# Kernel optimization log

Hardware: AMD Instinct MI355X
Metric: run time of the kernel (lower is better)

Reference implementation:

```python
import jax, jax.numpy as jnp
import numpy as np

H = 16          # num heads
BUCKETS = 256   # position_buckets -> pos_ebd_size (att_span)
MAX_REL = 512   # max_relative_positions


def _log_bucket(rel, bucket_size, max_position):
    mid = bucket_size // 2
    sign = jnp.sign(rel).astype(jnp.float32)
    abs_pos = jnp.where((rel < mid) & (rel > -mid), mid - 1, jnp.abs(rel)).astype(jnp.float32)
    log_pos = jnp.ceil(jnp.log(abs_pos / mid) / np.log((max_position - 1) / mid) * (mid - 1)) + mid
    bucket = jnp.where(abs_pos <= mid, rel.astype(jnp.float32), log_pos * sign)
    return bucket.astype(jnp.int32)


def _rel_pos(seq_len):
    ids = jnp.arange(seq_len)
    rel = ids[:, None] - ids[None, :]
    return _log_bucket(rel, BUCKETS, MAX_REL)  # [S,S] int32 in [-span, span]


def setup_inputs() -> dict:
    key = jax.random.key(0)
    ks = jax.random.split(key, 16)
    B, S, D = 4, 1024, 1024
    K2 = 2 * BUCKETS
    s = 0.02
    def lin(k, din, dout):
        return jax.random.normal(k, (din, dout), jnp.float32) * s
    return {
        "hidden_states": jax.random.normal(ks[0], (B, S, D), jnp.float32),
        "Wq": lin(ks[1], D, D), "bq": jnp.zeros((D,), jnp.float32),
        "Wk": lin(ks[2], D, D), "bk": jnp.zeros((D,), jnp.float32),
        "Wv": lin(ks[3], D, D), "bv": jnp.zeros((D,), jnp.float32),
        "Wo": lin(ks[4], D, D), "bo": jnp.zeros((D,), jnp.float32),
        "rel_emb": jax.random.normal(ks[5], (K2, D), jnp.float32) * s,
        "ln_g": jnp.ones((D,), jnp.float32), "ln_b": jnp.zeros((D,), jnp.float32),
        "Wpk": lin(ks[6], D, D), "bpk": jnp.zeros((D,), jnp.float32),
        "Wpq": lin(ks[7], D, D), "bpq": jnp.zeros((D,), jnp.float32),
    }


def reference(hidden_states, Wq, bq, Wk, bk, Wv, bv, Wo, bo,
              rel_emb, ln_g, ln_b, Wpk, bpk, Wpq, bpq):
    B, S, D = hidden_states.shape
    hd = D // H
    span = BUCKETS

    def shape_heads(x):  # [*, L, D] -> [*, H, L, hd]
        return x.reshape(*x.shape[:-1], H, hd).swapaxes(-2, -3)

    q = shape_heads(hidden_states @ Wq + bq)  # [B,H,S,hd]
    k = shape_heads(hidden_states @ Wk + bk)
    v = shape_heads(hidden_states @ Wv + bv)

    scale_factor = 3  # 1 + c2p + p2c
    scores = jnp.einsum('bhsd,bhkd->bhsk', q, k) / jnp.sqrt(jnp.float32(hd * scale_factor))

    # relative embeddings: LayerNorm over feature dim
    mu = rel_emb.mean(-1, keepdims=True)
    var = rel_emb.var(-1, keepdims=True)
    re = (rel_emb - mu) / jnp.sqrt(var + 1e-5) * ln_g + ln_b  # [2K, D]

    pos_k = shape_heads(re @ Wpk + bpk)  # [H, 2K, hd]
    pos_q = shape_heads(re @ Wpq + bpq)  # [H, 2K, hd]

    rel = _rel_pos(S)  # [S,S]
    bias_scale = jnp.sqrt(jnp.float32(hd * 2))

    # content-to-position
    c2p = jnp.einsum('bhsd,hkd->bhsk', q, pos_k)  # [B,H,S,2K]
    c2p_idx = jnp.clip(rel + span, 0, 2 * span - 1)  # [S,S]
    c2p = jnp.take_along_axis(c2p, jnp.broadcast_to(c2p_idx[None, None], (B, H, S, S)), axis=-1)
    scores = scores + c2p / bias_scale

    # position-to-content
    p2c = jnp.einsum('bhsd,hkd->bhsk', k, pos_q)  # [B,H,S,2K]
    p2c_idx = jnp.clip(-rel + span, 0, 2 * span - 1)
    p2c = jnp.take_along_axis(p2c, jnp.broadcast_to(p2c_idx[None, None], (B, H, S, S)), axis=-1)
    scores = scores + p2c.swapaxes(-1, -2) / bias_scale

    probs = jax.nn.softmax(scores.astype(jnp.float32), axis=-1).astype(q.dtype)
    ctx = jnp.einsum('bhsk,bhkd->bhsd', probs, v)  # [B,H,S,hd]
    ctx = ctx.swapaxes(1, 2).reshape(B, S, D)
    return ctx @ Wo + bo
```

## Files before the change

kernel.cpp:

```cpp
#include <hip/hip_runtime.h>

typedef unsigned short u16;
typedef __attribute__((ext_vector_type(8))) short short8_t;
typedef __attribute__((ext_vector_type(4))) float floatx4;

typedef const void __attribute__((address_space(1)))* gas_ptr;
typedef void __attribute__((address_space(3)))* las_ptr;

__device__ __forceinline__ float bf2f(u16 u){
  union { unsigned i; float f; } v; v.i = ((unsigned)u) << 16; return v.f;
}
__device__ __forceinline__ u16 f2bf(float x){
  unsigned u = __float_as_uint(x);
  return (u16)((u + 0x7FFFu + ((u >> 16) & 1u)) >> 16);
}
__device__ __forceinline__ int bucket_idx(int delta){
  int b;
  if (delta >= -128 && delta <= 128) b = delta;
  else {
    float a = (float)(delta < 0 ? -delta : delta);
    float lp = ceilf(logf(a * (1.0f / 128.0f)) / logf(511.0f / 128.0f) * 127.0f) + 128.0f;
    b = (int)lp;
    if (delta < 0) b = -b;
  }
  int idx = b + 256;
  return idx < 0 ? 0 : (idx > 511 ? 511 : idx);
}
__device__ __forceinline__ int win_lo(int s0, int t){
  int dlo = s0 - t * 64 - 63;
  int lo = bucket_idx(dlo) & ~1;
  return lo > 384 ? 384 : lo;
}

__global__ __launch_bounds__(256) void k_prep(
    const float* __restrict__ hs,
    const float* __restrict__ W0, const float* __restrict__ W1, const float* __restrict__ W2,
    const float* __restrict__ W3, const float* __restrict__ W4, const float* __restrict__ W5,
    const float* __restrict__ rel, const float* __restrict__ lng, const float* __restrict__ lnb,
    const float* __restrict__ bq, const float* __restrict__ bk, const float* __restrict__ bv,
    const float* __restrict__ bpk, const float* __restrict__ bpq,
    u16* __restrict__ h_bf, u16* __restrict__ Wt5, u16* __restrict__ Wo_t,
    u16* __restrict__ re_bf, u16* __restrict__ idxt,
    float* __restrict__ qkvb, float* __restrict__ posb)
{
  __shared__ float t[64][65];
  const int bid = blockIdx.x, tid = threadIdx.x;
  if (bid < 4096){
    int i = bid * 256 + tid;
    float4 v = ((const float4*)hs)[i];
    ushort4 o;
    o.x = f2bf(v.x); o.y = f2bf(v.y); o.z = f2bf(v.z); o.w = f2bf(v.w);
    ((ushort4*)h_bf)[i] = o;
  } else if (bid < 5632){
    int b2 = bid - 4096;
    int z = b2 >> 8, rem = b2 & 255;
    const float* W = (z == 0) ? W0 : (z == 1) ? W1 : (z == 2) ? W2 : (z == 3) ? W3 : (z == 4) ? W4 : W5;
    u16* Wt = (z < 5) ? (Wt5 + (long)z * 1048576) : Wo_t;
    int n0 = (rem & 15) * 64, k0 = (rem >> 4) * 64;
    #pragma unroll
    for (int i = 0; i < 16; i++){
      int e = i * 256 + tid; int r = e >> 6, c = e & 63;
      t[r][c] = W[(long)(k0 + r) * 1024 + n0 + c];
    }
    __syncthreads();
    #pragma unroll
    for (int i = 0; i < 16; i++){
      int e = i * 256 + tid; int r = e >> 6, c = e & 63;
      Wt[(long)(n0 + r) * 1024 + k0 + c] = f2bf(t[c][r]);
    }
  } else if (bid < 6144){
    int row = bid - 5632;
    float* red = (float*)t;
    float4 v = ((const float4*)(rel + (long)row * 1024))[tid];
    float s  = v.x + v.y + v.z + v.w;
    float s2 = v.x*v.x + v.y*v.y + v.z*v.z + v.w*v.w;
    #pragma unroll
    for (int o = 1; o < 64; o <<= 1){ s += __shfl_xor(s, o); s2 += __shfl_xor(s2, o); }
    if ((tid & 63) == 0){ red[(tid >> 6) * 2] = s; red[(tid >> 6) * 2 + 1] = s2; }
    __syncthreads();
    s  = red[0] + red[2] + red[4] + red[6];
    s2 = red[1] + red[3] + red[5] + red[7];
    float mu  = s * (1.f / 1024.f);
    float var = s2 * (1.f / 1024.f) - mu * mu;
    float rs  = rsqrtf(var + 1e-5f);
    float4 gg = ((const float4*)lng)[tid];
    float4 bb = ((const float4*)lnb)[tid];
    ushort4 o;
    o.x = f2bf((v.x - mu) * rs * gg.x + bb.x);
    o.y = f2bf((v.y - mu) * rs * gg.y + bb.y);
    o.z = f2bf((v.z - mu) * rs * gg.z + bb.z);
    o.w = f2bf((v.w - mu) * rs * gg.w + bb.w);
    ((ushort4*)(re_bf + (long)row * 1024))[tid] = o;
  } else {
    for (int i = tid; i < 2048; i += 256)
      idxt[i] = (u16)bucket_idx(i - 1024);
    for (int i = tid; i < 1024; i += 256){
      qkvb[i] = bq[i]; qkvb[1024 + i] = bk[i]; qkvb[2048 + i] = bv[i];
      posb[i] = bpk[i]; posb[1024 + i] = bpq[i];
    }
  }
}

template<int MODE>
__global__ __launch_bounds__(256) void k_gemm(
    const u16* __restrict__ A, const u16* __restrict__ Bt,
    const float* __restrict__ bias, void* __restrict__ C, void* __restrict__ C2,
    int M, int N, int K, int lda, int ldb)
{
  __shared__ __attribute__((aligned(16))) u16 smem[16384];
  u16* As = smem;
  u16* Bs = smem + 8192;
  const int z = blockIdx.z;
  const u16* Ab = A;
  const u16* Bb = Bt;
  if (MODE == 3){ Bb = Bt + (long)z * 1048576; bias += z << 10; }
  if (MODE == 4){ Ab = A + (long)z * 65536; Bb = Bt + (long)(z >> 6) * 524288 + (long)(z & 15) * 32768; }
  const int m0 = blockIdx.y * 128, n0 = blockIdx.x * 128;
  const int tid = threadIdx.x, lane = tid & 63, w = tid >> 6;
  const int wm = (w >> 1) * 64, wn = (w & 1) * 64;
  floatx4 acc[4][4];
  #pragma unroll
  for (int i = 0; i < 4; i++)
    #pragma unroll
    for (int j = 0; j < 4; j++) acc[i][j] = (floatx4){0.f, 0.f, 0.f, 0.f};

  const int r8 = lane >> 3;
  const int cswz = ((lane & 7) ^ r8) << 4;

  for (int kt = 0; kt < K; kt += 64){
    #pragma unroll
    for (int c = 0; c < 4; c++){
      int row = (c * 4 + w) * 8 + r8;
      const char* ga = (const char*)(Ab + (long)(m0 + row) * lda + kt) + cswz;
      __builtin_amdgcn_global_load_lds((gas_ptr)ga, (las_ptr)((char*)As + (c * 4 + w) * 1024), 16, 0, 0);
      const char* gb = (const char*)(Bb + (long)(n0 + row) * ldb + kt) + cswz;
      __builtin_amdgcn_global_load_lds((gas_ptr)gb, (las_ptr)((char*)Bs + (c * 4 + w) * 1024), 16, 0, 0);
    }
    __syncthreads();
    short8_t af[2][4], bfr[2][4];
    #pragma unroll
    for (int kk = 0; kk < 2; kk++){
      #pragma unroll
      for (int i = 0; i < 4; i++){
        int ra = wm + i * 16 + (lane & 15);
        af[kk][i] = *(const short8_t*)((const char*)As + ra * 128 + ((kk * 64 + ((lane >> 4) << 4)) ^ ((ra & 7) << 4)));
        int rb = wn + i * 16 + (lane & 15);
        bfr[kk][i] = *(const short8_t*)((const char*)Bs + rb * 128 + ((kk * 64 + ((lane >> 4) << 4)) ^ ((rb & 7) << 4)));
      }
    }
    #pragma unroll
    for (int i = 0; i < 4; i++)
      #pragma unroll
      for (int j = 0; j < 4; j++){
        acc[i][j] = __builtin_amdgcn_mfma_f32_16x16x32_bf16(af[0][i], bfr[0][j], acc[i][j], 0, 0, 0);
        acc[i][j] = __builtin_amdgcn_mfma_f32_16x16x32_bf16(af[1][i], bfr[1][j], acc[i][j], 0, 0, 0);
      }
    __syncthreads();
  }

  if (MODE == 0){
    float* fs = (float*)smem;
    #pragma unroll
    for (int h = 0; h < 2; h++){
      if ((w & 1) == h){
        #pragma unroll
        for (int i = 0; i < 4; i++)
          #pragma unroll
          for (int j = 0; j < 4; j++)
            #pragma unroll
            for (int r = 0; r < 4; r++){
              int ml = wm + i * 16 + ((lane >> 4) << 2) + r;
              int nl = j * 16 + (lane & 15);
              fs[ml * 64 + (nl ^ (((ml >> 2) & 3) << 4))] = acc[i][j][r] + bias[n0 + h * 64 + nl];
            }
      }
      __syncthreads();
      const int row16 = tid >> 4, cch = tid & 15;
      #pragma unroll
      for (int rr = 0; rr < 8; rr++){
        int ml = rr * 16 + row16;
        float4 vv = *(const float4*)&fs[ml * 64 + ((cch * 4) ^ (((ml >> 2) & 3) << 4))];
        *(float4*)((float*)C + (long)(m0 + ml) * N + n0 + h * 64 + cch * 4) = vv;
      }
      __syncthreads();
    }
    return;
  }

  if (MODE == 4){
    #pragma unroll
    for (int i = 0; i < 4; i++){
      #pragma unroll
      for (int j = 0; j < 4; j++){
        #pragma unroll
        for (int r = 0; r < 4; r++){
          int ml = wm + i * 16 + ((lane >> 4) << 2) + r;
          int nl = wn + j * 16 + (lane & 15);
          int byte_ = ml * 256 + ((nl * 2) ^ ((ml & 7) << 4));
          *(u16*)((char*)smem + byte_) = f2bf(exp2f(acc[i][j][r] * 0.12751743f));
        }
      }
    }
    __syncthreads();
    const int row16 = tid >> 4, cch = tid & 15;
    #pragma unroll
    for (int rr = 0; rr < 8; rr++){
      int ml = rr * 16 + row16;
      short8_t vv = *(const short8_t*)((const char*)smem + ml * 256 + ((cch * 16) ^ ((ml & 7) << 4)));
      *(short8_t*)((u16*)C + (long)z * 524288 + (long)(m0 + ml) * 512 + n0 + cch * 8) = vv;
    }
    return;
  }

  if (MODE == 5){
    if (n0 >= 2048){
      #pragma unroll
      for (int i = 0; i < 4; i++){
        #pragma unroll
        for (int j = 0; j < 4; j++){
          #pragma unroll
          for (int r = 0; r < 4; r++){
            int ml = wm + i * 16 + ((lane >> 4) << 2) + r;
            int nl = wn + j * 16 + (lane & 15);
            float v = acc[i][j][r] + bias[n0 + nl];
            int byte_ = nl * 256 + ((ml * 2) ^ ((nl & 7) << 4));
            *(u16*)((char*)smem + byte_) = f2bf(v);
          }
        }
      }
      __syncthreads();
      #pragma unroll
      for (int rr = 0; rr < 8; rr++){
        int nl = rr * 16 + (tid >> 4);
        int np = n0 + nl - 2048;
        int mc = tid & 15;
        short8_t vv = *(const short8_t*)((const char*)smem + nl * 256 + ((mc * 16) ^ ((nl & 7) << 4)));
        int m = m0 + mc * 8;
        long base = ((long)((m >> 10) * 16 + (np >> 6)) * 64 + (np & 63)) * 1024 + (m & 1023);
        *(short8_t*)((u16*)C2 + base) = vv;
      }
    } else {
      #pragma unroll
      for (int i = 0; i < 4; i++){
        #pragma unroll
        for (int j = 0; j < 4; j++){
          #pragma unroll
          for (int r = 0; r < 4; r++){
            int ml = wm + i * 16 + ((lane >> 4) << 2) + r;
            int nl = wn + j * 16 + (lane & 15);
            float v = acc[i][j][r] + bias[n0 + nl];
            int byte_ = ml * 256 + ((nl * 2) ^ ((ml & 7) << 4));
            *(u16*)((char*)smem + byte_) = f2bf(v);
          }
        }
      }
      __syncthreads();
      const int row16 = tid >> 4, cch = tid & 15;
      const int mat = n0 >> 10;
      u16* Cd = (u16*)C + (long)mat * 4194304;
      #pragma unroll
      for (int rr = 0; rr < 8; rr++){
        int ml = rr * 16 + row16;
        short8_t vv = *(const short8_t*)((const char*)smem + ml * 256 + ((cch * 16) ^ ((ml & 7) << 4)));
        int m = m0 + ml;
        int np = (n0 & 1023) + cch * 8;
        long base = ((long)((m >> 10) * 16 + (np >> 6)) * 1024 + (m & 1023)) * 64 + (np & 63);
        *(short8_t*)(Cd + base) = vv;
      }
    }
    return;
  }

  #pragma unroll
  for (int i = 0; i < 4; i++){
    #pragma unroll
    for (int j = 0; j < 4; j++){
      #pragma unroll
      for (int r = 0; r < 4; r++){
        int m = m0 + wm + i * 16 + ((lane >> 4) << 2) + r;
        int n = n0 + wn + j * 16 + (lane & 15);
        float v = acc[i][j][r] + bias[n];
        ((u16*)C)[(long)z * 524288 + ((long)(n >> 6) * 512 + m) * 64 + (n & 63)] = f2bf(v);
      }
    }
  }
}

__global__ __launch_bounds__(256, 2) void k_bias(
    const u16* __restrict__ EC, const u16* __restrict__ EP,
    const u16* __restrict__ T3, u16* __restrict__ EB, int bhbase)
{
  __shared__ __attribute__((aligned(16))) u16 C2W[2][8192];
  __shared__ __attribute__((aligned(16))) u16 P2W[2][8192];
  __shared__ __attribute__((aligned(16))) u16 IDW[2][128];
  const int flat0 = blockIdx.x;
  const int chunk = gridDim.x >> 3;
  const int flat = (flat0 & 7) * chunk + (flat0 >> 3);
  const int bhl = flat >> 5;
  const int sb  = (flat >> 1) & 15;
  const int kq  = flat & 1;
  const int bh = bhbase + bhl;
  const int tid = threadIdx.x, lane = tid & 63, w = tid >> 6;
  const int s0 = sb * 64;
  const u16* c2b = EC + (long)bh * 524288;
  const u16* p2b = EP + (long)bh * 524288;
  u16* EBb = EB + ((long)bhl << 20);

  const int r2 = tid >> 2;
  const int q2 = tid & 3;
  const int c2key = (r2 & 15) << 4;

  auto STAGE = [&](int buf, int t){
    const int ixlo = win_lo(s0, t);
    const int k0 = t * 64;
    #pragma unroll
    for (int r = 0; r < 16; r++){
      int row = w * 16 + r;
      const char* sa = (const char*)(c2b + (long)(s0 + row) * 512 + ixlo) + ((lane * 4) ^ ((row & 15) << 4));
      __builtin_amdgcn_global_load_lds((gas_ptr)sa, (las_ptr)((char*)&C2W[buf][0] + row * 256), 4, 0, 0);
      const char* sp = (const char*)(p2b + (long)(k0 + row) * 512 + ixlo) + ((lane * 4) ^ ((row & 15) << 4));
      __builtin_amdgcn_global_load_lds((gas_ptr)sp, (las_ptr)((char*)&P2W[buf][0] + row * 256), 4, 0, 0);
    }
    if (w == 3){
      int dev = s0 - k0 - 64;
      __builtin_amdgcn_global_load_lds((gas_ptr)((const char*)(T3 + (dev + 1024)) + lane * 4),
                                       (las_ptr)((char*)&IDW[buf][0]), 4, 0, 0);
    }
  };

  const int t0 = kq * 8;
  STAGE(0, t0);
  asm volatile("s_waitcnt vmcnt(0)" ::: "memory");
  __builtin_amdgcn_s_barrier();

  for (int i = 0; i < 8; i++){
    const int t = t0 + i, buf = i & 1;
    const int k0 = t * 64;
    const int ixlo = win_lo(s0, t);

    if (i < 7) STAGE(buf ^ 1, t + 1);

    u16 ov[16];
    #pragma unroll
    for (int c = 0; c < 16; c++){
      int kl = q2 * 16 + c;
      int j = r2 - kl + 64;
      int ix = (int)IDW[buf][j];
      int x = (ix - ixlo) * 2;
      float b1 = bf2f(*(const u16*)((const char*)&C2W[buf][0] + r2 * 256 + (x ^ c2key)));
      float b2 = bf2f(*(const u16*)((const char*)&P2W[buf][0] + kl * 256 + (x ^ ((kl & 15) << 4))));
      ov[c] = f2bf(b1 * b2);
    }
    u16* dst = EBb + (((long)(s0 + r2)) << 10) + k0 + q2 * 16;
    uint4 st0, st1;
    st0.x = (unsigned)ov[0]  | ((unsigned)ov[1]  << 16);
    st0.y = (unsigned)ov[2]  | ((unsigned)ov[3]  << 16);
    st0.z = (unsigned)ov[4]  | ((unsigned)ov[5]  << 16);
    st0.w = (unsigned)ov[6]  | ((unsigned)ov[7]  << 16);
    st1.x = (unsigned)ov[8]  | ((unsigned)ov[9]  << 16);
    st1.y = (unsigned)ov[10] | ((unsigned)ov[11] << 16);
    st1.z = (unsigned)ov[12] | ((unsigned)ov[13] << 16);
    st1.w = (unsigned)ov[14] | ((unsigned)ov[15] << 16);
    *(uint4*)dst = st0;
    *(uint4*)(dst + 8) = st1;

    if (i < 7){
      asm volatile("s_waitcnt vmcnt(2)" ::: "memory");
      __builtin_amdgcn_s_barrier();
    }
  }
}

__global__ __launch_bounds__(256, 3) void k_attn_eb(
    const u16* __restrict__ Q, const u16* __restrict__ K, const u16* __restrict__ Vt,
    const u16* __restrict__ EB, u16* __restrict__ ctx, int bhbase)
{
  __shared__ __attribute__((aligned(16))) u16 Ks[2][4096];
  __shared__ __attribute__((aligned(16))) u16 Vs[2][4096];
  __shared__ __attribute__((aligned(16))) u16 EBs[4096];
  __shared__ __attribute__((aligned(16))) u16 Pt[4096];
  const int flat0 = blockIdx.x;
  const int chunk = gridDim.x >> 3;
  const int flat = (flat0 & 7) * chunk + (flat0 >> 3);
  const int bhl = flat >> 4, sb = flat & 15;
  const int bh = bhbase + bhl;
  const int tid = threadIdx.x, lane = tid & 63, w = tid >> 6;
  const int s15 = lane & 15, g = lane >> 4;
  const int s0 = sb * 64;
  const int myrow = w * 16 + s15;
  const int s_row = s0 + myrow;
  const u16* Qb  = Q   + (long)bh * 65536;
  const u16* Kg  = K   + (long)bh * 65536;
  const u16* Vg  = Vt  + (long)bh * 65536;
  const u16* EBg = EB  + ((long)bhl << 20);

  short8_t qf0 = *(const short8_t*)(Qb + (long)s_row * 64 + g * 8);
  short8_t qf1 = *(const short8_t*)(Qb + (long)s_row * 64 + 32 + g * 8);

  const int srow8  = lane >> 3;
  const int schunk = (lane & 7) ^ srow8;
  const float sA2 = 0.10411754f;

  auto STAGE_KV = [&](int buf, int kt){
    #pragma unroll
    for (int ii = 0; ii < 2; ii++){
      int i = w * 2 + ii;
      int row = i * 8 + srow8;
      __builtin_amdgcn_global_load_lds(
        (gas_ptr)((const char*)(Kg + (long)(kt + row) * 64) + schunk * 16),
        (las_ptr)((char*)&Ks[buf][0] + i * 1024), 16, 0, 0);
      __builtin_amdgcn_global_load_lds(
        (gas_ptr)((const char*)(Vg + (long)row * 1024 + kt) + schunk * 16),
        (las_ptr)((char*)&Vs[buf][0] + i * 1024), 16, 0, 0);
    }
  };
  auto STAGE_EB = [&](int kt){
    #pragma unroll
    for (int ii = 0; ii < 2; ii++){
      int rowl = w * 16 + ii * 8 + srow8;
      const char* src = (const char*)(EBg + (((long)(s0 + rowl)) << 10) + kt) + schunk * 16;
      __builtin_amdgcn_global_load_lds((gas_ptr)src,
        (las_ptr)((char*)EBs + (w * 2 + ii) * 1024), 16, 0, 0);
    }
  };

  STAGE_KV(0, 0);
  STAGE_EB(0);

  float rowsum = 0.f;
  floatx4 oacc[4];
  #pragma unroll
  for (int dt = 0; dt < 4; dt++) oacc[dt] = (floatx4){0.f, 0.f, 0.f, 0.f};

  const int psw = (myrow & 7) << 4;

  for (int t = 0; t < 16; t++){
    const int buf = t & 1;
    const int kt = t * 64;

    asm volatile("s_waitcnt vmcnt(2)" ::: "memory");
    asm volatile("s_waitcnt lgkmcnt(0)" ::: "memory");
    __builtin_amdgcn_s_barrier();

    STAGE_KV(buf ^ 1, (t < 15) ? kt + 64 : 0);

    floatx4 a[4];
    #pragma unroll
    for (int T = 0; T < 4; T++){
      int row = T * 16 + s15;
      const char* rp = (const char*)&Ks[buf][0] + row * 128;
      int sw = (row & 7) << 4;
      short8_t k0v = *(const short8_t*)(rp + ((g * 16) ^ sw));
      short8_t k1v = *(const short8_t*)(rp + ((64 + g * 16) ^ sw));
      floatx4 acc = (floatx4){0.f, 0.f, 0.f, 0.f};
      acc = __builtin_amdgcn_mfma_f32_16x16x32_bf16(k0v, qf0, acc, 0, 0, 0);
      acc = __builtin_amdgcn_mfma_f32_16x16x32_bf16(k1v, qf1, acc, 0, 0, 0);
      a[T] = acc;
    }

    asm volatile("s_waitcnt vmcnt(4)" ::: "memory");

    #pragma unroll
    for (int T = 0; T < 4; T++){
      uint2 ebv = *(const uint2*)((const char*)EBs + myrow * 128 + ((T * 32 + g * 8) ^ psw));
      float e0 = exp2f(a[T][0] * sA2) * bf2f((u16)(ebv.x & 0xffff));
      float e1 = exp2f(a[T][1] * sA2) * bf2f((u16)(ebv.x >> 16));
      float e2 = exp2f(a[T][2] * sA2) * bf2f((u16)(ebv.y & 0xffff));
      float e3 = exp2f(a[T][3] * sA2) * bf2f((u16)(ebv.y >> 16));
      u16 p0 = f2bf(e0), p1 = f2bf(e1), p2v = f2bf(e2), p3 = f2bf(e3);
      rowsum += (bf2f(p0) + bf2f(p1)) + (bf2f(p2v) + bf2f(p3));
      uint2 pk2;
      pk2.x = (unsigned)p0  | ((unsigned)p1 << 16);
      pk2.y = (unsigned)p2v | ((unsigned)p3 << 16);
      *(uint2*)((char*)Pt + myrow * 128 + ((T * 32 + g * 8) ^ psw)) = pk2;
    }

    asm volatile("s_waitcnt lgkmcnt(0)" ::: "memory");
    STAGE_EB((t < 15) ? kt + 64 : 0);

    #pragma unroll
    for (int M = 0; M < 2; M++){
      short8_t pf = *(const short8_t*)((const char*)Pt + myrow * 128 + ((M * 64 + g * 16) ^ psw));
      #pragma unroll
      for (int dt = 0; dt < 4; dt++){
        int drow = dt * 16 + s15;
        short8_t vf = *(const short8_t*)((const char*)&Vs[buf][0] + drow * 128 + ((M * 64 + g * 16) ^ ((drow & 7) << 4)));
        oacc[dt] = __builtin_amdgcn_mfma_f32_16x16x32_bf16(pf, vf, oacc[dt], 0, 0, 0);
      }
    }
  }

  asm volatile("s_waitcnt vmcnt(0)" ::: "memory");

  rowsum += __shfl_xor(rowsum, 16);
  rowsum += __shfl_xor(rowsum, 32);
  float rinv = 1.f / rowsum;

  const int b = bh >> 4, h = bh & 15;
  #pragma unroll
  for (int r = 0; r < 4; r++){
    float ri = __shfl(rinv, g * 4 + r);
    int s_out = s0 + w * 16 + g * 4 + r;
    #pragma unroll
    for (int dt = 0; dt < 4; dt++){
      long oi = ((long)b * 1024 + s_out) * 1024 + h * 64 + dt * 16 + s15;
      ctx[oi] = f2bf(oacc[dt][r] * ri);
    }
  }
}

extern "C" void kernel_launch(void* const* d_in, const int* in_sizes, int n_in,
                              void* d_out, int out_size, void* d_ws, size_t ws_size,
                              hipStream_t stream){
  const float* hs  = (const float*)d_in[0];
  const float* Wq  = (const float*)d_in[1];
  const float* bq  = (const float*)d_in[2];
  const float* Wk  = (const float*)d_in[3];
  const float* bk  = (const float*)d_in[4];
  const float* Wv  = (const float*)d_in[5];
  const float* bv  = (const float*)d_in[6];
  const float* Wo  = (const float*)d_in[7];
  const float* bo  = (const float*)d_in[8];
  const float* rel = (const float*)d_in[9];
  const float* lng = (const float*)d_in[10];
  const float* lnb = (const float*)d_in[11];
  const float* Wpk = (const float*)d_in[12];
  const float* bpk = (const float*)d_in[13];
  const float* Wpq = (const float*)d_in[14];
  const float* bpq = (const float*)d_in[15];

  char* ws = (char*)d_ws;
  size_t off = 0;
  auto alloc = [&](size_t bytes){ size_t o = off; off += (bytes + 255) & ~(size_t)255; return o; };
  u16* Wo_t  = (u16*)(ws + alloc(1048576UL * 2));
  u16* Qd    = (u16*)(ws + alloc(4194304UL * 2));
  u16* Kd    = (u16*)(ws + alloc(4194304UL * 2));
  u16* Vtd   = (u16*)(ws + alloc(4194304UL * 2));
  u16* ECd   = (u16*)(ws + alloc(33554432UL * 2));
  u16* EPd   = (u16*)(ws + alloc(33554432UL * 2));
  u16* ctx   = (u16*)(ws + alloc(4194304UL * 2));
  u16* idxt  = (u16*)(ws + alloc(2048UL * 2));
  float* qkvb = (float*)(ws + alloc(3072UL * 4));
  float* posb = (float*)(ws + alloc(2048UL * 4));
  size_t dead0 = off;
  u16* h_bf  = (u16*)(ws + alloc(4194304UL * 2));
  u16* Wt5   = (u16*)(ws + alloc(5UL * 1048576 * 2));
  u16* re_bf = (u16*)(ws + alloc(524288UL * 2));
  u16* posk  = (u16*)(ws + alloc(524288UL * 2));
  u16* posq  = (u16*)(ws + alloc(524288UL * 2));
  u16* EB    = (u16*)(ws + dead0);
  const bool full = (ws_size >= dead0 + 134217728UL);
  (void)posq; (void)Kd;

  k_prep<<<6145, 256, 0, stream>>>(hs, Wq, Wk, Wv, Wpk, Wpq, Wo, rel, lng, lnb,
                                   bq, bk, bv, bpk, bpq,
                                   h_bf, Wt5, Wo_t, re_bf, idxt, qkvb, posb);

  k_gemm<5><<<dim3(24, 32, 1), 256, 0, stream>>>(h_bf, Wt5, qkvb, Qd, Vtd,
                                                 4096, 3072, 1024, 1024, 1024);
  k_gemm<3><<<dim3(8, 4, 2), 256, 0, stream>>>(re_bf, Wt5 + 3145728, posb, posk, nullptr,
                                               512, 1024, 1024, 1024, 1024);
  k_gemm<4><<<dim3(4, 8, 128), 256, 0, stream>>>(Qd, posk, nullptr, ECd, nullptr,
                                                 1024, 512, 64, 64, 64);

  if (full){
    k_bias   <<<dim3(2048), 256, 0, stream>>>(ECd, EPd, idxt, EB, 0);
    k_attn_eb<<<dim3(1024), 256, 0, stream>>>(Qd, Kd, Vtd, EB, ctx, 0);
  } else {
    k_bias   <<<dim3(1024), 256, 0, stream>>>(ECd, EPd, idxt, EB, 0);
    k_attn_eb<<<dim3(512),  256, 0, stream>>>(Qd, Kd, Vtd, EB, ctx, 0);
    k_bias   <<<dim3(1024), 256, 0, stream>>>(ECd, EPd, idxt, EB, 32);
    k_attn_eb<<<dim3(512),  256, 0, stream>>>(Qd, Kd, Vtd, EB, ctx, 32);
  }

  k_gemm<0><<<dim3(8, 32, 1), 256, 0, stream>>>(ctx, Wo_t, bo, d_out, nullptr,
                                                4096, 1024, 1024, 1024, 1024);
}
```

Before: 277.9 us.

## Fuse positional projection GEMM into QKV GEMM launch and remap tile order

The separate launch for the relative-embedding projection (pos_k/pos_q) is folded into the QKV projection kernel by adding extra grid rows that take the positional path, with surplus blocks exiting early. This removes one kernel launch and lets the small positional GEMM fill idle CUs alongside the large GEMM. The QKV and output-projection GEMMs also remap block IDs into a strided order meant to improve L2 locality across XCDs. Risks: the added branching and early-exit blocks, plus a different tile ordering that could change cache behaviour.

```diff
diff --git a/kernel.cpp b/kernel.cpp
--- a/kernel.cpp
+++ b/kernel.cpp
@@ -105,17 +105,46 @@
 __global__ __launch_bounds__(256) void k_gemm(
     const u16* __restrict__ A, const u16* __restrict__ Bt,
     const float* __restrict__ bias, void* __restrict__ C, void* __restrict__ C2,
-    int M, int N, int K, int lda, int ldb)
+    int M, int N, int K, int lda, int ldb,
+    const u16* __restrict__ Apos, const float* __restrict__ biaspos, void* __restrict__ Cpos)
 {
   __shared__ __attribute__((aligned(16))) u16 smem[16384];
   u16* As = smem;
   u16* Bs = smem + 8192;
+  const int bx = blockIdx.x, by = blockIdx.y;
   const int z = blockIdx.z;
   const u16* Ab = A;
   const u16* Bb = Bt;
-  if (MODE == 3){ Bb = Bt + (long)z * 1048576; bias += z << 10; }
-  if (MODE == 4){ Ab = A + (long)z * 65536; Bb = Bt + (long)(z >> 6) * 524288 + (long)(z & 15) * 32768; }
-  const int m0 = blockIdx.y * 128, n0 = blockIdx.x * 128;
+  const float* biasv = bias;
+  bool pospath = false;
+  int pz = 0;
+  int m0, n0;
+  if (MODE == 5){
+    if (by >= 32){
+      if (bx >= 16) return;
+      pospath = true;
+      pz = bx >> 3;
+      Ab = Apos;
+      Bb = Bt + 3145728 + (long)pz * 1048576;
+      biasv = biaspos + (pz << 10);
+      m0 = (by - 32) * 128;
+      n0 = (bx & 7) * 128;
+    } else {
+      int bid = by * 24 + bx;
+      int nf = (bid & 7) * 96 + (bid >> 3);
+      m0 = (nf / 24) * 128;
+      n0 = (nf % 24) * 128;
+    }
+  } else if (MODE == 0){
+    int bid = by * 8 + bx;
+    int nf = (bid & 7) * 32 + (bid >> 3);
+    m0 = (nf >> 3) * 128;
+    n0 = (nf & 7) * 128;
+  } else {
+    if (MODE == 4){ Ab = A + (long)z * 65536; Bb = Bt + (long)(z >> 6) * 524288 + (long)(z & 15) * 32768; }
+    m0 = by * 128;
+    n0 = bx * 128;
+  }
   const int tid = threadIdx.x, lane = tid & 63, w = tid >> 6;
   const int wm = (w >> 1) * 64, wn = (w & 1) * 64;
   floatx4 acc[4][4];
@@ -171,7 +200,7 @@
             for (int r = 0; r < 4; r++){
               int ml = wm + i * 16 + ((lane >> 4) << 2) + r;
               int nl = j * 16 + (lane & 15);
-              fs[ml * 64 + (nl ^ (((ml >> 2) & 3) << 4))] = acc[i][j][r] + bias[n0 + h * 64 + nl];
+              fs[ml * 64 + (nl ^ (((ml >> 2) & 3) << 4))] = acc[i][j][r] + biasv[n0 + h * 64 + nl];
             }
       }
       __syncthreads();
@@ -213,6 +242,22 @@
   }
 
   if (MODE == 5){
+    if (pospath){
+      #pragma unroll
+      for (int i = 0; i < 4; i++){
+        #pragma unroll
+        for (int j = 0; j < 4; j++){
+          #pragma unroll
+          for (int r = 0; r < 4; r++){
+            int m = m0 + wm + i * 16 + ((lane >> 4) << 2) + r;
+            int n = n0 + wn + j * 16 + (lane & 15);
+            float v = acc[i][j][r] + biasv[n];
+            ((u16*)Cpos)[(long)pz * 524288 + ((long)(n >> 6) * 512 + m) * 64 + (n & 63)] = f2bf(v);
+          }
+        }
+      }
+      return;
+    }
     if (n0 >= 2048){
       #pragma unroll
       for (int i = 0; i < 4; i++){
@@ -222,7 +267,7 @@
           for (int r = 0; r < 4; r++){
             int ml = wm + i * 16 + ((lane >> 4) << 2) + r;
             int nl = wn + j * 16 + (lane & 15);
-            float v = acc[i][j][r] + bias[n0 + nl];
+            float v = acc[i][j][r] + biasv[n0 + nl];
             int byte_ = nl * 256 + ((ml * 2) ^ ((nl & 7) << 4));
             *(u16*)((char*)smem + byte_) = f2bf(v);
           }
@@ -248,7 +293,7 @@
           for (int r = 0; r < 4; r++){
             int ml = wm + i * 16 + ((lane >> 4) << 2) + r;
             int nl = wn + j * 16 + (lane & 15);
-            float v = acc[i][j][r] + bias[n0 + nl];
+            float v = acc[i][j][r] + biasv[n0 + nl];
             int byte_ = ml * 256 + ((nl * 2) ^ ((ml & 7) << 4));
             *(u16*)((char*)smem + byte_) = f2bf(v);
           }
@@ -269,20 +314,6 @@
       }
     }
     return;
-  }
-
-  #pragma unroll
-  for (int i = 0; i < 4; i++){
-    #pragma unroll
-    for (int j = 0; j < 4; j++){
-      #pragma unroll
-      for (int r = 0; r < 4; r++){
-        int m = m0 + wm + i * 16 + ((lane >> 4) << 2) + r;
-        int n = n0 + wn + j * 16 + (lane & 15);
-        float v = acc[i][j][r] + bias[n];
-        ((u16*)C)[(long)z * 524288 + ((long)(n >> 6) * 512 + m) * 64 + (n & 63)] = f2bf(v);
-      }
-    }
   }
 }
 
@@ -556,12 +587,12 @@
                                    bq, bk, bv, bpk, bpq,
                                    h_bf, Wt5, Wo_t, re_bf, idxt, qkvb, posb);
 
-  k_gemm<5><<<dim3(24, 32, 1), 256, 0, stream>>>(h_bf, Wt5, qkvb, Qd, Vtd,
-                                                 4096, 3072, 1024, 1024, 1024);
-  k_gemm<3><<<dim3(8, 4, 2), 256, 0, stream>>>(re_bf, Wt5 + 3145728, posb, posk, nullptr,
-                                               512, 1024, 1024, 1024, 1024);
+  k_gemm<5><<<dim3(24, 36, 1), 256, 0, stream>>>(h_bf, Wt5, qkvb, Qd, Vtd,
+                                                 4096, 3072, 1024, 1024, 1024,
+                                                 re_bf, posb, posk);
   k_gemm<4><<<dim3(4, 8, 128), 256, 0, stream>>>(Qd, posk, nullptr, ECd, nullptr,
-                                                 1024, 512, 64, 64, 64);
+                                                 1024, 512, 64, 64, 64,
+                                                 nullptr, nullptr, nullptr);
 
   if (full){
     k_bias   <<<dim3(2048), 256, 0, stream>>>(ECd, EPd, idxt, EB, 0);
@@ -574,5 +605,6 @@
   }
 
   k_gemm<0><<<dim3(8, 32, 1), 256, 0, stream>>>(ctx, Wo_t, bo, d_out, nullptr,
-                                                4096, 1024, 1024, 1024, 1024);
-}
+                                                4096, 1024, 1024, 1024, 1024,
+                                                nullptr, nullptr, nullptr);
+}
```

Measured after the change: 258.8 us. -6.9%, faster.
